# Performance work log

Hardware: AMD Instinct MI355X
Metric: run time of the kernel (lower is better)

The kernel has to match this reference:

```python
import jax, jax.numpy as jnp
import numpy as np

# Mixtral-style config (scaled)
L = 2          # num_hidden_layers
H = 1024       # hidden_size
NH = 16        # num_attention_heads
KVH = 4        # num_key_value_heads
HD = H // NH   # head_dim = 64
F = 1024       # intermediate_size (per expert)
E = 8          # num_local_experts
K = 2          # num_experts_per_tok
EPS = 1e-5     # rms_norm_eps
THETA = 1e6    # rope_theta
B, S = 1, 2048


def setup_inputs() -> dict:
    key = jax.random.key(0)
    ks = jax.random.split(key, 10)
    s = 0.02
    inputs_embeds = jax.random.normal(ks[0], (B, S, H), jnp.float32)
    ln1 = jnp.ones((L, H), jnp.float32)
    ln2 = jnp.ones((L, H), jnp.float32)
    final_ln = jnp.ones((H,), jnp.float32)
    q_w = jax.random.normal(ks[1], (L, NH * HD, H), jnp.float32) * s
    k_w = jax.random.normal(ks[2], (L, KVH * HD, H), jnp.float32) * s
    v_w = jax.random.normal(ks[3], (L, KVH * HD, H), jnp.float32) * s
    o_w = jax.random.normal(ks[4], (L, H, NH * HD), jnp.float32) * s
    gate_w = jax.random.normal(ks[5], (L, E, H), jnp.float32) * s
    w1 = jax.random.normal(ks[6], (L, E, F, H), jnp.float32) * s
    w2 = jax.random.normal(ks[7], (L, E, H, F), jnp.float32) * s
    w3 = jax.random.normal(ks[8], (L, E, F, H), jnp.float32) * s
    return {"inputs_embeds": inputs_embeds, "ln1": ln1, "ln2": ln2,
            "final_ln": final_ln, "q_w": q_w, "k_w": k_w, "v_w": v_w,
            "o_w": o_w, "gate_w": gate_w, "w1": w1, "w2": w2, "w3": w3}


def _rmsnorm(x, w):
    v = jnp.mean(jnp.square(x), axis=-1, keepdims=True)
    return (x * jax.lax.rsqrt(v + EPS)) * w


def _rotate_half(x):
    x1, x2 = jnp.split(x, 2, axis=-1)
    return jnp.concatenate([-x2, x1], axis=-1)


def _rope_tables():
    inv_freq = 1.0 / (THETA ** (jnp.arange(0, HD, 2, dtype=jnp.float32) / HD))
    t = jnp.arange(S, dtype=jnp.float32)
    freqs = jnp.outer(t, inv_freq)              # [S, HD/2]
    emb = jnp.concatenate([freqs, freqs], -1)   # [S, HD]
    return jnp.cos(emb), jnp.sin(emb)


def _attn(x, qw, kw, vw, ow, cos, sin, mask):
    q = (x @ qw.T).reshape(B, S, NH, HD).transpose(0, 2, 1, 3)    # [B,NH,S,D]
    k = (x @ kw.T).reshape(B, S, KVH, HD).transpose(0, 2, 1, 3)   # [B,KVH,S,D]
    v = (x @ vw.T).reshape(B, S, KVH, HD).transpose(0, 2, 1, 3)
    q = q * cos + _rotate_half(q) * sin
    k = k * cos + _rotate_half(k) * sin
    rep = NH // KVH
    k = jnp.repeat(k, rep, axis=1)   # GQA expand -> [B,NH,S,D]
    v = jnp.repeat(v, rep, axis=1)
    scores = jnp.einsum('bhqd,bhkd->bhqk', q, k) / jnp.sqrt(jnp.float32(HD))
    scores = jnp.where(mask, scores, jnp.finfo(scores.dtype).min)
    p = jax.nn.softmax(scores, axis=-1)
    o = jnp.einsum('bhqk,bhkd->bhqd', p, v)
    o = o.transpose(0, 2, 1, 3).reshape(B, S, NH * HD)
    return o @ ow.T


def _moe(x, gw, w1_l, w2_l, w3_l):
    xf = x.reshape(-1, H)                                   # [T,H]
    T = xf.shape[0]
    logits = xf @ gw.T                                      # [T,E]
    probs = jax.nn.softmax(logits, axis=-1)
    topw, topi = jax.lax.top_k(probs, K)                    # [T,K]
    topw = topw / jnp.sum(topw, axis=-1, keepdims=True)
    wfull = jnp.zeros((T, E), probs.dtype).at[jnp.arange(T)[:, None], topi].set(topw)
    g = jnp.einsum('th,efh->tef', xf, w1_l)                 # [T,E,F]
    u = jnp.einsum('th,efh->tef', xf, w3_l)
    a = jax.nn.silu(g) * u
    y = jnp.einsum('te,tef,ehf->th', wfull, a, w2_l)
    return y.reshape(x.shape)


def reference(inputs_embeds, ln1, ln2, final_ln, q_w, k_w, v_w, o_w, gate_w, w1, w2, w3):
    cos, sin = _rope_tables()
    mask = jnp.tril(jnp.ones((S, S), bool))[None, None]     # causal
    h = inputs_embeds
    for l in range(L):
        h = h + _attn(_rmsnorm(h, ln1[l]), q_w[l], k_w[l], v_w[l], o_w[l], cos, sin, mask)
        h = h + _moe(_rmsnorm(h, ln2[l]), gate_w[l], w1[l], w2[l], w3[l])
    return _rmsnorm(h, final_ln)
```

## Files before the change

kernel.cpp:

```cpp
#include <hip/hip_runtime.h>
#include <hip/hip_bf16.h>
#include <math.h>

#define S_LEN 2048
#define HID   1024
#define NHEAD 16
#define KVH   4
#define HD    64
#define FF    1024
#define NE    8
#define NL    2
#define NSLOT 144

#define OFF_H    0
#define OFF_Q    (OFF_H + S_LEN*HID)
#define OFF_K    (OFF_Q + S_LEN*HID)
#define OFF_V    (OFF_K + S_LEN*KVH*HD)
#define OFF_COS  (OFF_V + S_LEN*KVH*HD)
#define OFF_SIN  (OFF_COS + S_LEN*32)
#define OFF_WT   (OFF_SIN + S_LEN*32)
#define OFF_INT  (OFF_WT + NE*S_LEN)
#define OFF_TOPE (OFF_INT + NE*S_LEN + 16)
#define OFF_TOPW (OFF_TOPE + S_LEN)
#define OFF_XH   (OFF_TOPW + 2*S_LEN)
#define OFF_AOH  (OFF_XH + S_LEN*HID/2)
#define OFF_ABH  (OFF_AOH + S_LEN*HID/2)
#define OFF_Q16  (OFF_ABH + NE*S_LEN*FF/2)
#define OFF_K16  (OFF_Q16 + S_LEN*HID/2)
#define OFF_VT16 (OFF_K16 + S_LEN*KVH*HD/2)
#define OFF_PO   (OFF_VT16 + S_LEN*KVH*HD/2)
#define OFF_PM   (OFF_PO + NSLOT*NHEAD*64*64)
#define OFF_PL   (OFF_PM + NSLOT*NHEAD*64)
#define OFF_WCVT (OFF_PL + NSLOT*NHEAD*64)

typedef __attribute__((ext_vector_type(8))) _Float16 f16x8;
typedef __attribute__((ext_vector_type(8))) short  s16x8;
typedef __attribute__((ext_vector_type(4))) float  f32x4;

__device__ __forceinline__ short f2h(float f) {
    union { _Float16 h; short s; } u;
    u.h = (_Float16)f;
    return u.s;
}

__device__ __forceinline__ s16x8 cvt8(float4 a, float4 b) {
    s16x8 w;
    w[0]=f2h(a.x); w[1]=f2h(a.y); w[2]=f2h(a.z); w[3]=f2h(a.w);
    w[4]=f2h(b.x); w[5]=f2h(b.y); w[6]=f2h(b.z); w[7]=f2h(b.w);
    return w;
}

__global__ __launch_bounds__(256) void cvt16_kernel(const float* __restrict__ src,
                                                    short* __restrict__ dst, int n8) {
    int gid = blockIdx.x * 256 + threadIdx.x;
    if (gid >= n8) return;
    const float4* s = (const float4*)src + (size_t)gid * 2;
    *(s16x8*)(dst + (size_t)gid * 8) = cvt8(s[0], s[1]);
}

__global__ void rope_tables_kernel(float* __restrict__ cosb, float* __restrict__ sinb) {
    int gid = blockIdx.x * 256 + threadIdx.x;
    int t = gid >> 5, i = gid & 31;
    float invf = powf(1.0e6f, -(float)i / 32.0f);
    float ang = (float)t * invf;
    cosb[gid] = cosf(ang);
    sinb[gid] = sinf(ang);
}

__global__ __launch_bounds__(256) void rmsnorm_h16_kernel(const float* __restrict__ x,
                                                          const float* __restrict__ w,
                                                          short* __restrict__ oh) {
    int row = blockIdx.x;
    const float4* xr = (const float4*)(x + (size_t)row * HID);
    float4 xv = xr[threadIdx.x];
    float ss = xv.x*xv.x + xv.y*xv.y + xv.z*xv.z + xv.w*xv.w;
    for (int off = 32; off; off >>= 1) ss += __shfl_xor(ss, off);
    __shared__ float sred[4];
    if ((threadIdx.x & 63) == 0) sred[threadIdx.x >> 6] = ss;
    __syncthreads();
    float tot = sred[0] + sred[1] + sred[2] + sred[3];
    float scale = rsqrtf(tot * (1.0f / (float)HID) + 1e-5f);
    float4 wv = ((const float4*)w)[threadIdx.x];
    float4 o;
    o.x = xv.x * scale * wv.x; o.y = xv.y * scale * wv.y;
    o.z = xv.z * scale * wv.z; o.w = xv.w * scale * wv.w;
    union { short s[4]; float2 f2; } hh;
    hh.s[0]=f2h(o.x); hh.s[1]=f2h(o.y); hh.s[2]=f2h(o.z); hh.s[3]=f2h(o.w);
    ((float2*)(oh + (size_t)row * HID))[threadIdx.x] = hh.f2;
}

__global__ __launch_bounds__(256) void rmsnorm_gate_kernel(const float* __restrict__ x,
                                                           const float* __restrict__ w,
                                                           const float* __restrict__ gw,
                                                           short* __restrict__ oh,
                                                           int* __restrict__ tope,
                                                           float2* __restrict__ topw) {
    int row = blockIdx.x;
    const float4* xr = (const float4*)(x + (size_t)row * HID);
    float4 xv = xr[threadIdx.x];
    float ss = xv.x*xv.x + xv.y*xv.y + xv.z*xv.z + xv.w*xv.w;
    for (int off = 32; off; off >>= 1) ss += __shfl_xor(ss, off);
    __shared__ float sred[4];
    __shared__ float gred[4][NE];
    if ((threadIdx.x & 63) == 0) sred[threadIdx.x >> 6] = ss;
    __syncthreads();
    float tot = sred[0] + sred[1] + sred[2] + sred[3];
    float scale = rsqrtf(tot * (1.0f / (float)HID) + 1e-5f);
    float4 wv = ((const float4*)w)[threadIdx.x];
    float4 o;
    o.x = xv.x * scale * wv.x; o.y = xv.y * scale * wv.y;
    o.z = xv.z * scale * wv.z; o.w = xv.w * scale * wv.w;
    union { short s[4]; float2 f2; } hh;
    hh.s[0]=f2h(o.x); hh.s[1]=f2h(o.y); hh.s[2]=f2h(o.z); hh.s[3]=f2h(o.w);
    ((float2*)(oh + (size_t)row * HID))[threadIdx.x] = hh.f2;
    const float4* gr = (const float4*)gw;
    float acc[NE];
    #pragma unroll
    for (int e = 0; e < NE; ++e) {
        float4 g4 = gr[e * 256 + threadIdx.x];
        acc[e] = o.x*g4.x + o.y*g4.y + o.z*g4.z + o.w*g4.w;
    }
    #pragma unroll
    for (int e = 0; e < NE; ++e)
        for (int off = 32; off; off >>= 1) acc[e] += __shfl_xor(acc[e], off);
    if ((threadIdx.x & 63) == 0) {
        #pragma unroll
        for (int e = 0; e < NE; ++e) gred[threadIdx.x >> 6][e] = acc[e];
    }
    __syncthreads();
    if (threadIdx.x == 0) {
        float lg[NE];
        #pragma unroll
        for (int e = 0; e < NE; ++e)
            lg[e] = gred[0][e] + gred[1][e] + gred[2][e] + gred[3][e];
        float mx = lg[0];
        #pragma unroll
        for (int e = 1; e < NE; ++e) mx = fmaxf(mx, lg[e]);
        float p[NE];
        #pragma unroll
        for (int e = 0; e < NE; ++e) p[e] = __expf(lg[e] - mx);
        int i0 = 0;
        #pragma unroll
        for (int e = 1; e < NE; ++e) if (p[e] > p[i0]) i0 = e;
        int i1 = -1;
        #pragma unroll
        for (int e = 0; e < NE; ++e) if (e != i0 && (i1 < 0 || p[e] > p[i1])) i1 = e;
        float w0 = p[i0], w1 = p[i1];
        float inv = 1.0f / (w0 + w1);
        tope[row] = i0 | (i1 << 8);
        topw[row] = make_float2(w0 * inv, w1 * inv);
    }
}

__global__ __launch_bounds__(1024) void route_build_kernel(const int* __restrict__ tope,
                                                           const float2* __restrict__ topw,
                                                           int* __restrict__ cnt,
                                                           int* __restrict__ idx,
                                                           float* __restrict__ wt) {
    const int e = blockIdx.x;
    const int lane = threadIdx.x & 63, wv = threadIdx.x >> 6;
    __shared__ int wtot[16];
    __shared__ int sbase;
    if (threadIdx.x == 0) sbase = 0;
    __syncthreads();
    for (int t0 = 0; t0 < S_LEN; t0 += 1024) {
        int t = t0 + threadIdx.x;
        int pk = tope[t];
        int e0 = pk & 0xff, e1 = (pk >> 8) & 0xff;
        bool sel = (e0 == e) || (e1 == e);
        unsigned long long mask = __ballot(sel);
        int prefix = __popcll(mask & ((1ULL << lane) - 1ULL));
        if (lane == 0) wtot[wv] = __popcll(mask);
        __syncthreads();
        if (sel) {
            int off = sbase;
            for (int i = 0; i < wv; ++i) off += wtot[i];
            float2 wpair = topw[t];
            float wsel = (e0 == e) ? wpair.x : wpair.y;
            int slot = off + prefix;
            idx[e * S_LEN + slot] = t;
            wt[e * S_LEN + slot] = wsel;
        }
        __syncthreads();
        if (threadIdx.x == 0) {
            int s = 0;
            #pragma unroll
            for (int i = 0; i < 16; ++i) s += wtot[i];
            sbase += s;
        }
    }
    __syncthreads();
    if (threadIdx.x == 0) cnt[e] = sbase;
}

__global__ __launch_bounds__(256) void rmsnorm_kernel(const float* __restrict__ x,
                                                      const float* __restrict__ w,
                                                      float* __restrict__ out) {
    int row = blockIdx.x;
    const float4* xr = (const float4*)(x + (size_t)row * HID);
    float4 xv = xr[threadIdx.x];
    float ss = xv.x*xv.x + xv.y*xv.y + xv.z*xv.z + xv.w*xv.w;
    for (int off = 32; off; off >>= 1) ss += __shfl_xor(ss, off);
    __shared__ float sred[4];
    if ((threadIdx.x & 63) == 0) sred[threadIdx.x >> 6] = ss;
    __syncthreads();
    float tot = sred[0] + sred[1] + sred[2] + sred[3];
    float scale = rsqrtf(tot * (1.0f / (float)HID) + 1e-5f);
    float4 wv = ((const float4*)w)[threadIdx.x];
    float4 o;
    o.x = xv.x * scale * wv.x; o.y = xv.y * scale * wv.y;
    o.z = xv.z * scale * wv.z; o.w = xv.w * scale * wv.w;
    ((float4*)(out + (size_t)row * HID))[threadIdx.x] = o;
}

__global__ void rope_cvt_kernel(const float* __restrict__ p, const float* __restrict__ cosb,
                                const float* __restrict__ sinb, short* __restrict__ o16,
                                int nh, int total, float qscale) {
    int gid = blockIdx.x * 256 + threadIdx.x;
    if (gid >= total) return;
    int per = nh * 32;
    int t = gid / per, r = gid % per;
    int hh = r >> 5, i = r & 31;
    float c = cosb[t*32 + i], s = sinb[t*32 + i];
    const float* base = p + (size_t)t * (nh * HD) + hh * HD + i;
    float a = base[0], b = base[32];
    short* ob = o16 + (size_t)t * (nh * HD) + hh * HD + i;
    ob[0]  = f2h((a * c - b * s) * qscale);
    ob[32] = f2h((b * c + a * s) * qscale);
}

__global__ __launch_bounds__(256) void vtrans_kernel(const float* __restrict__ vb,
                                                     short* __restrict__ vt16) {
    __shared__ float tile[64][65];
    const int t0 = blockIdx.x * 64, d0 = blockIdx.y * 64;
    const int tr = threadIdx.x >> 2;
    const int dc = (threadIdx.x & 3) * 16;
    const float4* src = (const float4*)(vb + (size_t)(t0 + tr) * (KVH*HD) + d0 + dc);
    float4 v0 = src[0], v1 = src[1], v2 = src[2], v3 = src[3];
    tile[tr][dc+ 0]=v0.x; tile[tr][dc+ 1]=v0.y; tile[tr][dc+ 2]=v0.z; tile[tr][dc+ 3]=v0.w;
    tile[tr][dc+ 4]=v1.x; tile[tr][dc+ 5]=v1.y; tile[tr][dc+ 6]=v1.z; tile[tr][dc+ 7]=v1.w;
    tile[tr][dc+ 8]=v2.x; tile[tr][dc+ 9]=v2.y; tile[tr][dc+10]=v2.z; tile[tr][dc+11]=v2.w;
    tile[tr][dc+12]=v3.x; tile[tr][dc+13]=v3.y; tile[tr][dc+14]=v3.z; tile[tr][dc+15]=v3.w;
    __syncthreads();
    const int dr = threadIdx.x >> 2;
    const int tc = (threadIdx.x & 3) * 16;
    s16x8 w0, w1;
    #pragma unroll
    for (int i = 0; i < 8; ++i) {
        w0[i] = f2h(tile[tc + i][dr]);
        w1[i] = f2h(tile[tc + 8 + i][dr]);
    }
    short* dst = vt16 + (size_t)(d0 + dr) * S_LEN + t0 + tc;
    *(s16x8*)dst = w0;
    *(s16x8*)(dst + 8) = w1;
}

__device__ __forceinline__ void gemm64_core(
        const short* pA0, const short* pB0, const short* pB1,
        int Kd, int tid, short* As, short* Bs, f32x4 (&acc)[2][4]) {
    const int lane = tid & 63, lo = lane & 15, hi = lane >> 4;
    const int wid = tid >> 6, wr = wid >> 1, wc = wid & 1;
    const int srow = tid >> 2, scol = (tid & 3) * 8;
    s16x8 a0 = *(const s16x8*)pA0;
    s16x8 b0 = *(const s16x8*)pB0;
    s16x8 b1 = *(const s16x8*)pB1;
    *(s16x8*)&As[srow*40 + scol] = a0;
    *(s16x8*)&Bs[srow*40 + scol] = b0;
    *(s16x8*)&Bs[(64+srow)*40 + scol] = b1;
    __syncthreads();
    int p = 0;
    for (int k0 = 0; k0 < Kd; k0 += 32) {
        const bool more = (k0 + 32 < Kd);
        if (more) {
            a0 = *(const s16x8*)(pA0 + k0 + 32);
            b0 = *(const s16x8*)(pB0 + k0 + 32);
            b1 = *(const s16x8*)(pB1 + k0 + 32);
        }
        const short* Asp = As + p * (64*40);
        const short* Bsp = Bs + p * (128*40);
        f16x8 aF[2], bF[4];
        #pragma unroll
        for (int m = 0; m < 2; ++m) aF[m] = *(const f16x8*)&Asp[(wr*32 + m*16 + lo)*40 + hi*8];
        #pragma unroll
        for (int n = 0; n < 4; ++n) bF[n] = *(const f16x8*)&Bsp[(wc*64 + n*16 + lo)*40 + hi*8];
        #pragma unroll
        for (int m = 0; m < 2; ++m)
            #pragma unroll
            for (int n = 0; n < 4; ++n)
                acc[m][n] = __builtin_amdgcn_mfma_f32_16x16x32_f16(aF[m], bF[n], acc[m][n], 0, 0, 0);
        if (more) {
            short* Asn = As + (p ^ 1) * (64*40);
            short* Bsn = Bs + (p ^ 1) * (128*40);
            *(s16x8*)&Asn[srow*40 + scol] = a0;
            *(s16x8*)&Bsn[srow*40 + scol] = b0;
            *(s16x8*)&Bsn[(64+srow)*40 + scol] = b1;
        }
        __syncthreads();
        p ^= 1;
    }
}

__global__ __launch_bounds__(256) void gemm_h16_kernel(const short* __restrict__ Ag,
        const short* __restrict__ Bg, float* __restrict__ C,
        const float* __restrict__ resid, int N, int Kd) {
    __shared__ __align__(16) short As[2*64*40], Bs[2*128*40];
    const int tid = threadIdx.x;
    const int lane = tid & 63, lo = lane & 15, hi = lane >> 4;
    const int wid = tid >> 6, wr = wid >> 1, wc = wid & 1;
    const int m0 = blockIdx.y * 64, n0 = blockIdx.x * 128;
    const int srow = tid >> 2, scol = (tid & 3) * 8;
    f32x4 acc[2][4];
    #pragma unroll
    for (int m = 0; m < 2; ++m)
        #pragma unroll
        for (int n = 0; n < 4; ++n) { acc[m][n][0]=0.f; acc[m][n][1]=0.f; acc[m][n][2]=0.f; acc[m][n][3]=0.f; }
    gemm64_core(Ag + (size_t)(m0+srow)*Kd + scol,
                Bg + (size_t)(n0+srow)*Kd + scol, Bg + (size_t)(n0+64+srow)*Kd + scol,
                Kd, tid, As, Bs, acc);
    #pragma unroll
    for (int m = 0; m < 2; ++m)
        #pragma unroll
        for (int n = 0; n < 4; ++n)
            #pragma unroll
            for (int r = 0; r < 4; ++r) {
                int row = m0 + wr*32 + m*16 + hi*4 + r;
                int col = n0 + wc*64 + n*16 + lo;
                float val = acc[m][n][r];
                if (resid) val += resid[(size_t)row * N + col];
                C[(size_t)row * N + col] = val;
            }
}

__global__ __launch_bounds__(256) void qkv_h16_kernel(const short* __restrict__ Xh,
        const short* __restrict__ qw16, const short* __restrict__ kw16,
        const short* __restrict__ vw16,
        float* __restrict__ qo, float* __restrict__ ko, float* __restrict__ vo) {
    __shared__ __align__(16) short As[2*64*40], Bs[2*128*40];
    const int bx = blockIdx.x;
    const short* Bp; float* Cp; int Nc, n0;
    if (bx < 8)       { Bp = qw16; Cp = qo; Nc = 1024; n0 = bx * 128; }
    else if (bx < 10) { Bp = kw16; Cp = ko; Nc = 256;  n0 = (bx - 8) * 128; }
    else              { Bp = vw16; Cp = vo; Nc = 256;  n0 = (bx - 10) * 128; }
    const int tid = threadIdx.x;
    const int lane = tid & 63, lo = lane & 15, hi = lane >> 4;
    const int wid = tid >> 6, wr = wid >> 1, wc = wid & 1;
    const int m0 = blockIdx.y * 64;
    const int srow = tid >> 2, scol = (tid & 3) * 8;
    f32x4 acc[2][4];
    #pragma unroll
    for (int m = 0; m < 2; ++m)
        #pragma unroll
        for (int n = 0; n < 4; ++n) { acc[m][n][0]=0.f; acc[m][n][1]=0.f; acc[m][n][2]=0.f; acc[m][n][3]=0.f; }
    gemm64_core(Xh + (size_t)(m0+srow)*HID + scol,
                Bp + (size_t)(n0+srow)*HID + scol, Bp + (size_t)(n0+64+srow)*HID + scol,
                HID, tid, As, Bs, acc);
    #pragma unroll
    for (int m = 0; m < 2; ++m)
        #pragma unroll
        for (int n = 0; n < 4; ++n)
            #pragma unroll
            for (int r = 0; r < 4; ++r) {
                int row = m0 + wr*32 + m*16 + hi*4 + r;
                int col = n0 + wc*64 + n*16 + lo;
                Cp[(size_t)row * Nc + col] = acc[m][n][r];
            }
}

__global__ __launch_bounds__(256) void attn_mfma_kernel(const short* __restrict__ q16,
                                                        const short* __restrict__ k16,
                                                        const short* __restrict__ vt16,
                                                        float* __restrict__ pO,
                                                        float* __restrict__ pm,
                                                        float* __restrict__ pl) {
    __shared__ __align__(16) short Ks[64][72];
    __shared__ __align__(16) short Vt[64][72];
    __shared__ __align__(16) short Ps[4][16][72];
    const int wid = threadIdx.x >> 6, lane = threadIdx.x & 63;
    const int lo = lane & 15, hi = lane >> 4;
    const int head = blockIdx.y;
    const int s = (NSLOT - 1) - blockIdx.x;
    int g = 0, base = 0;
    while (g < 7 && s >= base + 4 * (g + 1)) { base += 4 * (g + 1); ++g; }
    const int tt = s - base;
    const int qi = 4 * g + tt / (g + 1);
    const int c  = tt % (g + 1);
    const int t_beg = c * 4;
    const int t_end = min(t_beg + 4, qi + 1);
    const int q0 = qi * 64;
    const int kvh = head >> 2;

    f16x8 qf[2];
    {
        const short* qr = q16 + (size_t)(q0 + wid*16 + lo) * HID + head*HD;
        qf[0] = *(const f16x8*)(qr + hi*8);
        qf[1] = *(const f16x8*)(qr + 32 + hi*8);
    }

    f32x4 acc[4];
    float m[4], l[4];
    #pragma unroll
    for (int r = 0; r < 4; ++r) {
        m[r] = -1e30f; l[r] = 0.f;
        acc[0][r] = 0.f; acc[1][r] = 0.f; acc[2][r] = 0.f; acc[3][r] = 0.f;
    }

    const int skey = threadIdx.x >> 2;
    const int sdg  = (threadIdx.x & 3) * 16;

    s16x8 ka0, ka1, va0, va1;
    {
        const short* kr = k16 + (size_t)(t_beg*64 + skey)*(KVH*HD) + kvh*HD + sdg;
        ka0 = *(const s16x8*)kr; ka1 = *(const s16x8*)(kr + 8);
        const short* vr = vt16 + (size_t)(kvh*HD + skey)*S_LEN + t_beg*64 + sdg;
        va0 = *(const s16x8*)vr; va1 = *(const s16x8*)(vr + 8);
    }

    for (int t = t_beg; t < t_end; ++t) {
        __syncthreads();
        *(s16x8*)&Ks[skey][sdg]     = ka0;
        *(s16x8*)&Ks[skey][sdg + 8] = ka1;
        *(s16x8*)&Vt[skey][sdg]     = va0;
        *(s16x8*)&Vt[skey][sdg + 8] = va1;
        __syncthreads();
        if (t + 1 < t_end) {
            const short* kr = k16 + (size_t)((t+1)*64 + skey)*(KVH*HD) + kvh*HD + sdg;
            ka0 = *(const s16x8*)kr; ka1 = *(const s16x8*)(kr + 8);
            const short* vr = vt16 + (size_t)(kvh*HD + skey)*S_LEN + (t+1)*64 + sdg;
            va0 = *(const s16x8*)vr; va1 = *(const s16x8*)(vr + 8);
        }
        const int k0 = t * 64;
        f32x4 sc[4];
        #pragma unroll
        for (int f = 0; f < 4; ++f) {
            f32x4 sf; sf[0]=0.f; sf[1]=0.f; sf[2]=0.f; sf[3]=0.f;
            f16x8 bk0 = *(const f16x8*)&Ks[f*16 + lo][hi*8];
            sf = __builtin_amdgcn_mfma_f32_16x16x32_f16(qf[0], bk0, sf, 0, 0, 0);
            f16x8 bk1 = *(const f16x8*)&Ks[f*16 + lo][32 + hi*8];
            sf = __builtin_amdgcn_mfma_f32_16x16x32_f16(qf[1], bk1, sf, 0, 0, 0);
            sc[f] = sf;
        }
        if (t == qi) {
            int qrow = q0 + wid*16 + hi*4;
            #pragma unroll
            for (int f = 0; f < 4; ++f)
                #pragma unroll
                for (int r = 0; r < 4; ++r)
                    if (k0 + f*16 + lo > qrow + r) sc[f][r] = -1e30f;
        }
        float pmax[4];
        #pragma unroll
        for (int r = 0; r < 4; ++r) {
            float x = fmaxf(fmaxf(sc[0][r], sc[1][r]), fmaxf(sc[2][r], sc[3][r]));
            x = fmaxf(x, __shfl_xor(x, 1));
            x = fmaxf(x, __shfl_xor(x, 2));
            x = fmaxf(x, __shfl_xor(x, 4));
            x = fmaxf(x, __shfl_xor(x, 8));
            pmax[r] = x;
        }
        bool ok = (pmax[0] <= m[0] + 8.f) && (pmax[1] <= m[1] + 8.f) &&
                  (pmax[2] <= m[2] + 8.f) && (pmax[3] <= m[3] + 8.f);
        if (!__all(ok)) {
            #pragma unroll
            for (int r = 0; r < 4; ++r) {
                float mn = fmaxf(m[r], pmax[r]);
                float sc_ = __expf(m[r] - mn);
                m[r] = mn;
                l[r] *= sc_;
                acc[0][r] *= sc_; acc[1][r] *= sc_;
                acc[2][r] *= sc_; acc[3][r] *= sc_;
            }
        }
        float rs[4] = {0.f, 0.f, 0.f, 0.f};
        #pragma unroll
        for (int f = 0; f < 4; ++f)
            #pragma unroll
            for (int r = 0; r < 4; ++r) {
                float e = __expf(sc[f][r] - m[r]);
                rs[r] += e;
                Ps[wid][hi*4 + r][f*16 + lo] = f2h(e);
            }
        #pragma unroll
        for (int r = 0; r < 4; ++r) {
            float x = rs[r];
            x += __shfl_xor(x, 1); x += __shfl_xor(x, 2);
            x += __shfl_xor(x, 4); x += __shfl_xor(x, 8);
            l[r] += x;
        }
        asm volatile("s_waitcnt lgkmcnt(0)" ::: "memory");
        __builtin_amdgcn_sched_barrier(0);
        f16x8 pa0 = *(const f16x8*)&Ps[wid][lo][hi*8];
        f16x8 pa1 = *(const f16x8*)&Ps[wid][lo][32 + hi*8];
        #pragma unroll
        for (int f = 0; f < 4; ++f) {
            f32x4 o = acc[f];
            f16x8 v0 = *(const f16x8*)&Vt[f*16 + lo][hi*8];
            o = __builtin_amdgcn_mfma_f32_16x16x32_f16(pa0, v0, o, 0, 0, 0);
            f16x8 v1 = *(const f16x8*)&Vt[f*16 + lo][32 + hi*8];
            o = __builtin_amdgcn_mfma_f32_16x16x32_f16(pa1, v1, o, 0, 0, 0);
            acc[f] = o;
        }
    }
    const int pbase = head * NSLOT + s;
    float* po = pO + (size_t)pbase * 4096;
    #pragma unroll
    for (int r = 0; r < 4; ++r)
        #pragma unroll
        for (int f = 0; f < 4; ++f)
            po[(wid*16 + hi*4 + r) * 64 + f*16 + lo] = acc[f][r];
    if (lo == 0) {
        #pragma unroll
        for (int r = 0; r < 4; ++r) {
            pm[pbase*64 + wid*16 + hi*4 + r] = m[r];
            pl[pbase*64 + wid*16 + hi*4 + r] = l[r];
        }
    }
}

__global__ __launch_bounds__(256) void attn_combine_kernel(const float* __restrict__ pO,
        const float* __restrict__ pm, const float* __restrict__ pl,
        short* __restrict__ aoh) {
    const int qi = blockIdx.x, head = blockIdx.y;
    const int g = qi >> 2, rr = qi & 3;
    const int nch = g + 1;
    const int sbase = (g + 1) * (2 * g + rr);
    const int row = threadIdx.x >> 2;
    const int d0 = (threadIdx.x & 3) * 16;
    float mv[8], lv[8];
    float mx = -1e30f;
    #pragma unroll
    for (int cd = 0; cd < 8; ++cd) {
        if (cd < nch) {
            int p = head * NSLOT + sbase + cd;
            mv[cd] = pm[p * 64 + row];
            lv[cd] = pl[p * 64 + row];
            mx = fmaxf(mx, mv[cd]);
        } else { mv[cd] = -1e30f; lv[cd] = 0.f; }
    }
    float w[8];
    float lsum = 0.f;
    #pragma unroll
    for (int cd = 0; cd < 8; ++cd) {
        w[cd] = (cd < nch) ? __expf(mv[cd] - mx) : 0.f;
        lsum += w[cd] * lv[cd];
    }
    float inv = 1.0f / lsum;
    float o[16] = {};
    #pragma unroll
    for (int cd = 0; cd < 8; ++cd) {
        if (cd < nch) {
            const float4* po = (const float4*)(pO + ((size_t)(head * NSLOT + sbase + cd)) * 4096 + row * 64 + d0);
            float wc = w[cd] * inv;
            #pragma unroll
            for (int j = 0; j < 4; ++j) {
                float4 vv = po[j];
                o[j*4+0] += wc * vv.x; o[j*4+1] += wc * vv.y;
                o[j*4+2] += wc * vv.z; o[j*4+3] += wc * vv.w;
            }
        }
    }
    size_t outb = (size_t)(qi * 64 + row) * HID + head * HD + d0;
    s16x8 w0, w1;
    #pragma unroll
    for (int i = 0; i < 8; ++i) { w0[i] = f2h(o[i]); w1[i] = f2h(o[8+i]); }
    *(s16x8*)(aoh + outb) = w0;
    *(s16x8*)(aoh + outb + 8) = w1;
}

__global__ __launch_bounds__(256) void moe_mlp1_h16(const short* __restrict__ Xh,
        const short* __restrict__ W1h, const short* __restrict__ W3h,
        const int* __restrict__ cnt, const int* __restrict__ idx,
        short* __restrict__ abh) {
    int e = blockIdx.z;
    int ne = cnt[e];
    int m0 = blockIdx.y * 64;
    if (m0 >= ne) return;
    int f0 = blockIdx.x * 64;
    __shared__ __align__(16) short As[2*64*40];
    __shared__ __align__(16) short Gs[2*64*40], Us[2*64*40];
    __shared__ int rows[64];
    const int tid = threadIdx.x;
    if (tid < 64) {
        int slot = m0 + tid;
        rows[tid] = (slot < ne) ? idx[e * S_LEN + slot] : 0;
    }
    __syncthreads();
    const int lane = tid & 63, lo = lane & 15, hi = lane >> 4;
    const int wid = tid >> 6, wr = wid >> 1, wc = wid & 1;
    const int srow = tid >> 2, scol = (tid & 3) * 8;
    const short* pX0 = Xh + (size_t)rows[srow] * HID + scol;
    const short* p1 = W1h + ((size_t)e * FF + f0 + srow) * HID + scol;
    const short* p3 = W3h + ((size_t)e * FF + f0 + srow) * HID + scol;

    f32x4 ag[2][2], au[2][2];
    #pragma unroll
    for (int m = 0; m < 2; ++m)
        #pragma unroll
        for (int n = 0; n < 2; ++n) {
            ag[m][n][0]=0.f; ag[m][n][1]=0.f; ag[m][n][2]=0.f; ag[m][n][3]=0.f;
            au[m][n][0]=0.f; au[m][n][1]=0.f; au[m][n][2]=0.f; au[m][n][3]=0.f;
        }

    s16x8 a0 = *(const s16x8*)pX0;
    s16x8 g0 = *(const s16x8*)p1;
    s16x8 u0 = *(const s16x8*)p3;
    *(s16x8*)&As[srow*40 + scol] = a0;
    *(s16x8*)&Gs[srow*40 + scol] = g0;
    *(s16x8*)&Us[srow*40 + scol] = u0;
    __syncthreads();
    int p = 0;
    for (int k0 = 0; k0 < HID; k0 += 32) {
        const bool more = (k0 + 32 < HID);
        if (more) {
            a0 = *(const s16x8*)(pX0 + k0 + 32);
            g0 = *(const s16x8*)(p1 + k0 + 32);
            u0 = *(const s16x8*)(p3 + k0 + 32);
        }
        const short* Asp = As + p * (64*40);
        const short* Gsp = Gs + p * (64*40);
        const short* Usp = Us + p * (64*40);
        f16x8 aF[2], gF[2], uF[2];
        #pragma unroll
        for (int m = 0; m < 2; ++m) aF[m] = *(const f16x8*)&Asp[(wr*32 + m*16 + lo)*40 + hi*8];
        #pragma unroll
        for (int n = 0; n < 2; ++n) {
            gF[n] = *(const f16x8*)&Gsp[(wc*32 + n*16 + lo)*40 + hi*8];
            uF[n] = *(const f16x8*)&Usp[(wc*32 + n*16 + lo)*40 + hi*8];
        }
        #pragma unroll
        for (int m = 0; m < 2; ++m)
            #pragma unroll
            for (int n = 0; n < 2; ++n) {
                ag[m][n] = __builtin_amdgcn_mfma_f32_16x16x32_f16(aF[m], gF[n], ag[m][n], 0, 0, 0);
                au[m][n] = __builtin_amdgcn_mfma_f32_16x16x32_f16(aF[m], uF[n], au[m][n], 0, 0, 0);
            }
        if (more) {
            short* Asn = As + (p ^ 1) * (64*40);
            short* Gsn = Gs + (p ^ 1) * (64*40);
            short* Usn = Us + (p ^ 1) * (64*40);
            *(s16x8*)&Asn[srow*40 + scol] = a0;
            *(s16x8*)&Gsn[srow*40 + scol] = g0;
            *(s16x8*)&Usn[srow*40 + scol] = u0;
        }
        __syncthreads();
        p ^= 1;
    }
    #pragma unroll
    for (int m = 0; m < 2; ++m)
        #pragma unroll
        for (int n = 0; n < 2; ++n)
            #pragma unroll
            for (int r = 0; r < 4; ++r) {
                int slot = m0 + wr*32 + m*16 + hi*4 + r;
                if (slot >= ne) continue;
                float g = ag[m][n][r], u = au[m][n][r];
                float a = g * (1.0f / (1.0f + __expf(-g))) * u;
                abh[((size_t)e * S_LEN + slot) * FF + f0 + wc*32 + n*16 + lo] = f2h(a);
            }
}

__global__ __launch_bounds__(256) void moe_mlp2_h16(const short* __restrict__ abh,
        const short* __restrict__ W2h,
        const int* __restrict__ cnt, const int* __restrict__ idx,
        const float* __restrict__ wt, float* __restrict__ hbuf) {
    int e = blockIdx.z >> 1;
    int ks = blockIdx.z & 1;
    int ne = cnt[e];
    int m0 = blockIdx.y * 64;
    if (m0 >= ne) return;
    int n0 = blockIdx.x * 128;
    const int koff = ks * (FF / 2);
    __shared__ __align__(16) short As[2*64*40], Bs[2*128*40];
    const int tid = threadIdx.x;
    const int lane = tid & 63, lo = lane & 15, hi = lane >> 4;
    const int wid = tid >> 6, wr = wid >> 1, wc = wid & 1;
    const int srow = tid >> 2, scol = (tid & 3) * 8;
    f32x4 acc[2][4];
    #pragma unroll
    for (int m = 0; m < 2; ++m)
        #pragma unroll
        for (int n = 0; n < 4; ++n) { acc[m][n][0]=0.f; acc[m][n][1]=0.f; acc[m][n][2]=0.f; acc[m][n][3]=0.f; }
    gemm64_core(abh + ((size_t)e*S_LEN + m0 + srow)*FF + koff + scol,
                W2h + ((size_t)e*HID + n0 + srow)*FF + koff + scol,
                W2h + ((size_t)e*HID + n0 + 64 + srow)*FF + koff + scol,
                FF / 2, tid, As, Bs, acc);
    #pragma unroll
    for (int m = 0; m < 2; ++m) {
        #pragma unroll
        for (int r = 0; r < 4; ++r) {
            int slot = m0 + wr*32 + m*16 + hi*4 + r;
            if (slot >= ne) continue;
            int tok = idx[e * S_LEN + slot];
            float wv = wt[e * S_LEN + slot];
            #pragma unroll
            for (int n = 0; n < 4; ++n)
                atomicAdd(&hbuf[(size_t)tok * HID + n0 + wc*64 + n*16 + lo], acc[m][n][r] * wv);
        }
    }
}

extern "C" void kernel_launch(void* const* d_in, const int* in_sizes, int n_in,
                              void* d_out, int out_size, void* d_ws, size_t ws_size,
                              hipStream_t stream) {
    const float* emb = (const float*)d_in[0];
    const float* ln1 = (const float*)d_in[1];
    const float* ln2 = (const float*)d_in[2];
    const float* fln = (const float*)d_in[3];
    const float* qw  = (const float*)d_in[4];
    const float* kw  = (const float*)d_in[5];
    const float* vw  = (const float*)d_in[6];
    const float* ow  = (const float*)d_in[7];
    const float* gw  = (const float*)d_in[8];
    const float* w1  = (const float*)d_in[9];
    const float* w2  = (const float*)d_in[10];
    const float* w3  = (const float*)d_in[11];

    float* ws   = (float*)d_ws;
    float* h    = ws + OFF_H;
    float* q    = ws + OFF_Q;
    float* kb   = ws + OFF_K;
    float* vb   = ws + OFF_V;
    float* cosb = ws + OFF_COS;
    float* sinb = ws + OFF_SIN;
    float* wt   = ws + OFF_WT;
    int*   cnt  = (int*)(ws + OFF_INT);
    int*   idx  = cnt + 8;
    int*   tope = (int*)(ws + OFF_TOPE);
    float2* topw = (float2*)(ws + OFF_TOPW);
    short* xh   = (short*)(ws + OFF_XH);
    short* aoh  = (short*)(ws + OFF_AOH);
    short* abh  = (short*)(ws + OFF_ABH);
    short* q16  = (short*)(ws + OFF_Q16);
    short* k16  = (short*)(ws + OFF_K16);
    short* vt16 = (short*)(ws + OFF_VT16);
    float* pO   = ws + OFF_PO;
    float* pm   = ws + OFF_PM;
    float* pl   = ws + OFF_PL;
    short* WC   = (short*)(ws + OFF_WCVT);

    short* sq = WC;
    short* sk = sq + HID*HID;
    short* sv = sk + KVH*HD*HID;
    short* so = sv + KVH*HD*HID;
    short* s1 = so + HID*HID;
    short* s3 = s1 + (size_t)NE*FF*HID;
    short* s2 = s3 + (size_t)NE*FF*HID;

    hipMemcpyAsync(h, emb, (size_t)S_LEN * HID * sizeof(float), hipMemcpyDeviceToDevice, stream);
    rope_tables_kernel<<<S_LEN * 32 / 256, 256, 0, stream>>>(cosb, sinb);

    const int n8_qo = HID*HID/8, n8_kv = KVH*HD*HID/8, n8_w = NE*FF*HID/8;

    for (int l = 0; l < NL; ++l) {
        cvt16_kernel<<<n8_qo/256, 256, 0, stream>>>(qw + (size_t)l*HID*HID, sq, n8_qo);
        cvt16_kernel<<<n8_kv/256, 256, 0, stream>>>(kw + (size_t)l*KVH*HD*HID, sk, n8_kv);
        cvt16_kernel<<<n8_kv/256, 256, 0, stream>>>(vw + (size_t)l*KVH*HD*HID, sv, n8_kv);
        cvt16_kernel<<<n8_qo/256, 256, 0, stream>>>(ow + (size_t)l*HID*HID, so, n8_qo);

        rmsnorm_h16_kernel<<<S_LEN, 256, 0, stream>>>(h, ln1 + l * HID, xh);
        qkv_h16_kernel<<<dim3(12, 32), 256, 0, stream>>>(xh, sq, sk, sv, q, kb, vb);
        rope_cvt_kernel<<<(S_LEN * NHEAD * 32) / 256, 256, 0, stream>>>(q, cosb, sinb, q16, NHEAD, S_LEN * NHEAD * 32, 0.125f);
        rope_cvt_kernel<<<(S_LEN * KVH * 32) / 256, 256, 0, stream>>>(kb, cosb, sinb, k16, KVH, S_LEN * KVH * 32, 1.0f);
        vtrans_kernel<<<dim3(S_LEN/64, KVH*HD/64), 256, 0, stream>>>(vb, vt16);
        attn_mfma_kernel<<<dim3(NSLOT, NHEAD), 256, 0, stream>>>(q16, k16, vt16, pO, pm, pl);
        attn_combine_kernel<<<dim3(32, NHEAD), 256, 0, stream>>>(pO, pm, pl, aoh);
        gemm_h16_kernel<<<dim3(8, 32), 256, 0, stream>>>(aoh, so, h, h, HID, HID);

        rmsnorm_gate_kernel<<<S_LEN, 256, 0, stream>>>(h, ln2 + l * HID, gw + (size_t)l * NE * HID,
                                                       xh, tope, topw);
        route_build_kernel<<<NE, 1024, 0, stream>>>(tope, topw, cnt, idx, wt);

        cvt16_kernel<<<n8_w/256, 256, 0, stream>>>(w1 + (size_t)l*NE*FF*HID, s1, n8_w);
        cvt16_kernel<<<n8_w/256, 256, 0, stream>>>(w3 + (size_t)l*NE*FF*HID, s3, n8_w);
        moe_mlp1_h16<<<dim3(16, 32, 8), 256, 0, stream>>>(xh, s1, s3, cnt, idx, abh);

        cvt16_kernel<<<n8_w/256, 256, 0, stream>>>(w2 + (size_t)l*NE*HID*FF, s2, n8_w);
        moe_mlp2_h16<<<dim3(8, 32, 16), 256, 0, stream>>>(abh, s2, cnt, idx, wt, h);
    }
    rmsnorm_kernel<<<S_LEN, 256, 0, stream>>>(h, fln, (float*)d_out);
}
```

Measured before the change: 486.1 us.

## Deepen register prefetch to two k-tiles in dense and MoE up GEMM loops

Both the shared dense GEMM core and the MoE gate/up kernel now keep two k-steps of global loads in flight in registers, not one. The loop is unrolled by two, and each LDS store is issued before the MFMAs of the current tile. The aim is to hide more global memory latency behind the matrix compute. In exchange it uses more VGPRs, which may lower occupancy, and the ordering now relies on a single barrier per step.

Result: faster. 474.6 us (-2.4%).

```diff
diff --git a/kernel.cpp b/kernel.cpp
--- a/kernel.cpp
+++ b/kernel.cpp
@@ -261,42 +261,77 @@
     const int lane = tid & 63, lo = lane & 15, hi = lane >> 4;
     const int wid = tid >> 6, wr = wid >> 1, wc = wid & 1;
     const int srow = tid >> 2, scol = (tid & 3) * 8;
-    s16x8 a0 = *(const s16x8*)pA0;
-    s16x8 b0 = *(const s16x8*)pB0;
-    s16x8 b1 = *(const s16x8*)pB1;
-    *(s16x8*)&As[srow*40 + scol] = a0;
-    *(s16x8*)&Bs[srow*40 + scol] = b0;
-    *(s16x8*)&Bs[(64+srow)*40 + scol] = b1;
+    const int aoff = srow*40 + scol;
+    const int boff0 = srow*40 + scol, boff1 = (64+srow)*40 + scol;
+
+    s16x8 a0_, b00_, b10_;
+    s16x8 a1_, b01_, b11_;
+
+    a0_ = *(const s16x8*)pA0; b00_ = *(const s16x8*)pB0; b10_ = *(const s16x8*)pB1;
+    *(s16x8*)&As[aoff]  = a0_;
+    *(s16x8*)&Bs[boff0] = b00_;
+    *(s16x8*)&Bs[boff1] = b10_;
+    if (32 < Kd) { a0_ = *(const s16x8*)(pA0+32); b00_ = *(const s16x8*)(pB0+32); b10_ = *(const s16x8*)(pB1+32); }
+    if (64 < Kd) { a1_ = *(const s16x8*)(pA0+64); b01_ = *(const s16x8*)(pB0+64); b11_ = *(const s16x8*)(pB1+64); }
     __syncthreads();
     int p = 0;
-    for (int k0 = 0; k0 < Kd; k0 += 32) {
-        const bool more = (k0 + 32 < Kd);
-        if (more) {
-            a0 = *(const s16x8*)(pA0 + k0 + 32);
-            b0 = *(const s16x8*)(pB0 + k0 + 32);
-            b1 = *(const s16x8*)(pB1 + k0 + 32);
-        }
-        const short* Asp = As + p * (64*40);
-        const short* Bsp = Bs + p * (128*40);
-        f16x8 aF[2], bF[4];
-        #pragma unroll
-        for (int m = 0; m < 2; ++m) aF[m] = *(const f16x8*)&Asp[(wr*32 + m*16 + lo)*40 + hi*8];
-        #pragma unroll
-        for (int n = 0; n < 4; ++n) bF[n] = *(const f16x8*)&Bsp[(wc*64 + n*16 + lo)*40 + hi*8];
-        #pragma unroll
-        for (int m = 0; m < 2; ++m)
-            #pragma unroll
-            for (int n = 0; n < 4; ++n)
-                acc[m][n] = __builtin_amdgcn_mfma_f32_16x16x32_f16(aF[m], bF[n], acc[m][n], 0, 0, 0);
-        if (more) {
-            short* Asn = As + (p ^ 1) * (64*40);
-            short* Bsn = Bs + (p ^ 1) * (128*40);
-            *(s16x8*)&Asn[srow*40 + scol] = a0;
-            *(s16x8*)&Bsn[srow*40 + scol] = b0;
-            *(s16x8*)&Bsn[(64+srow)*40 + scol] = b1;
-        }
-        __syncthreads();
-        p ^= 1;
+    for (int k0 = 0; k0 < Kd; k0 += 64) {
+        {
+            if (k0 + 32 < Kd) {
+                short* Asn = As + (p ^ 1) * (64*40);
+                short* Bsn = Bs + (p ^ 1) * (128*40);
+                *(s16x8*)&Asn[aoff]  = a0_;
+                *(s16x8*)&Bsn[boff0] = b00_;
+                *(s16x8*)&Bsn[boff1] = b10_;
+            }
+            if (k0 + 96 < Kd) {
+                a0_  = *(const s16x8*)(pA0 + k0 + 96);
+                b00_ = *(const s16x8*)(pB0 + k0 + 96);
+                b10_ = *(const s16x8*)(pB1 + k0 + 96);
+            }
+            const short* Asp = As + p * (64*40);
+            const short* Bsp = Bs + p * (128*40);
+            f16x8 aF[2], bF[4];
+            #pragma unroll
+            for (int m = 0; m < 2; ++m) aF[m] = *(const f16x8*)&Asp[(wr*32 + m*16 + lo)*40 + hi*8];
+            #pragma unroll
+            for (int n = 0; n < 4; ++n) bF[n] = *(const f16x8*)&Bsp[(wc*64 + n*16 + lo)*40 + hi*8];
+            #pragma unroll
+            for (int m = 0; m < 2; ++m)
+                #pragma unroll
+                for (int n = 0; n < 4; ++n)
+                    acc[m][n] = __builtin_amdgcn_mfma_f32_16x16x32_f16(aF[m], bF[n], acc[m][n], 0, 0, 0);
+            __syncthreads();
+            p ^= 1;
+        }
+        if (k0 + 32 < Kd) {
+            if (k0 + 64 < Kd) {
+                short* Asn = As + (p ^ 1) * (64*40);
+                short* Bsn = Bs + (p ^ 1) * (128*40);
+                *(s16x8*)&Asn[aoff]  = a1_;
+                *(s16x8*)&Bsn[boff0] = b01_;
+                *(s16x8*)&Bsn[boff1] = b11_;
+            }
+            if (k0 + 128 < Kd) {
+                a1_  = *(const s16x8*)(pA0 + k0 + 128);
+                b01_ = *(const s16x8*)(pB0 + k0 + 128);
+                b11_ = *(const s16x8*)(pB1 + k0 + 128);
+            }
+            const short* Asp = As + p * (64*40);
+            const short* Bsp = Bs + p * (128*40);
+            f16x8 aF[2], bF[4];
+            #pragma unroll
+            for (int m = 0; m < 2; ++m) aF[m] = *(const f16x8*)&Asp[(wr*32 + m*16 + lo)*40 + hi*8];
+            #pragma unroll
+            for (int n = 0; n < 4; ++n) bF[n] = *(const f16x8*)&Bsp[(wc*64 + n*16 + lo)*40 + hi*8];
+            #pragma unroll
+            for (int m = 0; m < 2; ++m)
+                #pragma unroll
+                for (int n = 0; n < 4; ++n)
+                    acc[m][n] = __builtin_amdgcn_mfma_f32_16x16x32_f16(aF[m], bF[n], acc[m][n], 0, 0, 0);
+            __syncthreads();
+            p ^= 1;
+        }
     }
 }
 
@@ -587,6 +622,7 @@
     const int lane = tid & 63, lo = lane & 15, hi = lane >> 4;
     const int wid = tid >> 6, wr = wid >> 1, wc = wid & 1;
     const int srow = tid >> 2, scol = (tid & 3) * 8;
+    const int soff = srow*40 + scol;
     const short* pX0 = Xh + (size_t)rows[srow] * HID + scol;
     const short* p1 = W1h + ((size_t)e * FF + f0 + srow) * HID + scol;
     const short* p3 = W3h + ((size_t)e * FF + f0 + srow) * HID + scol;
@@ -600,49 +636,87 @@
             au[m][n][0]=0.f; au[m][n][1]=0.f; au[m][n][2]=0.f; au[m][n][3]=0.f;
         }
 
-    s16x8 a0 = *(const s16x8*)pX0;
-    s16x8 g0 = *(const s16x8*)p1;
-    s16x8 u0 = *(const s16x8*)p3;
-    *(s16x8*)&As[srow*40 + scol] = a0;
-    *(s16x8*)&Gs[srow*40 + scol] = g0;
-    *(s16x8*)&Us[srow*40 + scol] = u0;
+    s16x8 a0_, g0_, u0_;
+    s16x8 a1_, g1_, u1_;
+    a0_ = *(const s16x8*)pX0; g0_ = *(const s16x8*)p1; u0_ = *(const s16x8*)p3;
+    *(s16x8*)&As[soff] = a0_;
+    *(s16x8*)&Gs[soff] = g0_;
+    *(s16x8*)&Us[soff] = u0_;
+    a0_ = *(const s16x8*)(pX0+32); g0_ = *(const s16x8*)(p1+32); u0_ = *(const s16x8*)(p3+32);
+    a1_ = *(const s16x8*)(pX0+64); g1_ = *(const s16x8*)(p1+64); u1_ = *(const s16x8*)(p3+64);
     __syncthreads();
     int p = 0;
-    for (int k0 = 0; k0 < HID; k0 += 32) {
-        const bool more = (k0 + 32 < HID);
-        if (more) {
-            a0 = *(const s16x8*)(pX0 + k0 + 32);
-            g0 = *(const s16x8*)(p1 + k0 + 32);
-            u0 = *(const s16x8*)(p3 + k0 + 32);
-        }
-        const short* Asp = As + p * (64*40);
-        const short* Gsp = Gs + p * (64*40);
-        const short* Usp = Us + p * (64*40);
-        f16x8 aF[2], gF[2], uF[2];
-        #pragma unroll
-        for (int m = 0; m < 2; ++m) aF[m] = *(const f16x8*)&Asp[(wr*32 + m*16 + lo)*40 + hi*8];
-        #pragma unroll
-        for (int n = 0; n < 2; ++n) {
-            gF[n] = *(const f16x8*)&Gsp[(wc*32 + n*16 + lo)*40 + hi*8];
-            uF[n] = *(const f16x8*)&Usp[(wc*32 + n*16 + lo)*40 + hi*8];
-        }
-        #pragma unroll
-        for (int m = 0; m < 2; ++m)
+    for (int k0 = 0; k0 < HID; k0 += 64) {
+        {
+            if (k0 + 32 < HID) {
+                short* Asn = As + (p ^ 1) * (64*40);
+                short* Gsn = Gs + (p ^ 1) * (64*40);
+                short* Usn = Us + (p ^ 1) * (64*40);
+                *(s16x8*)&Asn[soff] = a0_;
+                *(s16x8*)&Gsn[soff] = g0_;
+                *(s16x8*)&Usn[soff] = u0_;
+            }
+            if (k0 + 96 < HID) {
+                a0_ = *(const s16x8*)(pX0 + k0 + 96);
+                g0_ = *(const s16x8*)(p1 + k0 + 96);
+                u0_ = *(const s16x8*)(p3 + k0 + 96);
+            }
+            const short* Asp = As + p * (64*40);
+            const short* Gsp = Gs + p * (64*40);
+            const short* Usp = Us + p * (64*40);
+            f16x8 aF[2], gF[2], uF[2];
+            #pragma unroll
+            for (int m = 0; m < 2; ++m) aF[m] = *(const f16x8*)&Asp[(wr*32 + m*16 + lo)*40 + hi*8];
             #pragma unroll
             for (int n = 0; n < 2; ++n) {
-                ag[m][n] = __builtin_amdgcn_mfma_f32_16x16x32_f16(aF[m], gF[n], ag[m][n], 0, 0, 0);
-                au[m][n] = __builtin_amdgcn_mfma_f32_16x16x32_f16(aF[m], uF[n], au[m][n], 0, 0, 0);
-            }
-        if (more) {
-            short* Asn = As + (p ^ 1) * (64*40);
-            short* Gsn = Gs + (p ^ 1) * (64*40);
-            short* Usn = Us + (p ^ 1) * (64*40);
-            *(s16x8*)&Asn[srow*40 + scol] = a0;
-            *(s16x8*)&Gsn[srow*40 + scol] = g0;
-            *(s16x8*)&Usn[srow*40 + scol] = u0;
-        }
-        __syncthreads();
-        p ^= 1;
+                gF[n] = *(const f16x8*)&Gsp[(wc*32 + n*16 + lo)*40 + hi*8];
+                uF[n] = *(const f16x8*)&Usp[(wc*32 + n*16 + lo)*40 + hi*8];
+            }
+            #pragma unroll
+            for (int m = 0; m < 2; ++m)
+                #pragma unroll
+                for (int n = 0; n < 2; ++n) {
+                    ag[m][n] = __builtin_amdgcn_mfma_f32_16x16x32_f16(aF[m], gF[n], ag[m][n], 0, 0, 0);
+                    au[m][n] = __builtin_amdgcn_mfma_f32_16x16x32_f16(aF[m], uF[n], au[m][n], 0, 0, 0);
+                }
+            __syncthreads();
+            p ^= 1;
+        }
+        {
+            if (k0 + 64 < HID) {
+                short* Asn = As + (p ^ 1) * (64*40);
+                short* Gsn = Gs + (p ^ 1) * (64*40);
+                short* Usn = Us + (p ^ 1) * (64*40);
+                *(s16x8*)&Asn[soff] = a1_;
+                *(s16x8*)&Gsn[soff] = g1_;
+                *(s16x8*)&Usn[soff] = u1_;
+            }
+            if (k0 + 128 < HID) {
+                a1_ = *(const s16x8*)(pX0 + k0 + 128);
+                g1_ = *(const s16x8*)(p1 + k0 + 128);
+                u1_ = *(const s16x8*)(p3 + k0 + 128);
+            }
+            const short* Asp = As + p * (64*40);
+            const short* Gsp = Gs + p * (64*40);
+            const short* Usp = Us + p * (64*40);
+            f16x8 aF[2], gF[2], uF[2];
+            #pragma unroll
+            for (int m = 0; m < 2; ++m) aF[m] = *(const f16x8*)&Asp[(wr*32 + m*16 + lo)*40 + hi*8];
+            #pragma unroll
+            for (int n = 0; n < 2; ++n) {
+                gF[n] = *(const f16x8*)&Gsp[(wc*32 + n*16 + lo)*40 + hi*8];
+                uF[n] = *(const f16x8*)&Usp[(wc*32 + n*16 + lo)*40 + hi*8];
+            }
+            #pragma unroll
+            for (int m = 0; m < 2; ++m)
+                #pragma unroll
+                for (int n = 0; n < 2; ++n) {
+                    ag[m][n] = __builtin_amdgcn_mfma_f32_16x16x32_f16(aF[m], gF[n], ag[m][n], 0, 0, 0);
+                    au[m][n] = __builtin_amdgcn_mfma_f32_16x16x32_f16(aF[m], uF[n], au[m][n], 0, 0, 0);
+                }
+            __syncthreads();
+            p ^= 1;
+        }
     }
     #pragma unroll
     for (int m = 0; m < 2; ++m)
```
